# Kernel optimization log

Hardware: AMD Instinct MI355X
Metric: run time of the kernel (lower is better)

## Reference

```python
import jax, jax.numpy as jnp
import numpy as np

LAM = 10.0          # lam_val from __init__ (cp.Constant)
N_ITERS = 100       # fixed FISTA iterations; converges to QP solution (kappa ~ 1+16*LAM)


def _dtd(v):
    """Apply D^T D where D is the (n-2, n) second-difference operator, along last axis."""
    d = v[..., 2:] - 2.0 * v[..., 1:-1] + v[..., :-2]            # D v, shape (..., n-2)
    pad = [(0, 0)] * (v.ndim - 1) + [(2, 2)]
    dp = jnp.pad(d, pad)                                          # zero-pad for adjoint
    return dp[..., 2:] - 2.0 * dp[..., 1:-1] + dp[..., :-2]      # D^T d, shape (..., n)


def _solve_rows(y):
    """Batched QP:  min ||y - x||^2 + LAM * ||diff(x, 2)||^2  s.t.  0 <= x <= y,
    solved independently along the last axis via projected accelerated gradient (FISTA).
    Hessian/2 = I + LAM * D^T D, lambda_max(D^T D) <= 16 -> Lipschitz L = 2*(1 + 16*LAM).
    """
    step = 1.0 / (2.0 * (1.0 + 16.0 * LAM))
    proj = lambda v: jnp.clip(v, 0.0, y)   # box projection onto [0, y]
    x0 = proj(y)

    def body(i, carry):
        x, z, t = carry
        g = 2.0 * (z - y) + (2.0 * LAM) * _dtd(z)
        x_new = proj(z - step * g)
        t_new = 0.5 * (1.0 + jnp.sqrt(1.0 + 4.0 * t * t))
        z_new = x_new + ((t - 1.0) / t_new) * (x_new - x)
        return (x_new, z_new, t_new)

    x, _, _ = jax.lax.fori_loop(0, N_ITERS, body, (x0, x0, jnp.float32(1.0)))
    return x


def setup_inputs() -> dict:
    key = jax.random.key(0)
    # Batch of images in [0,1] (like normalized MNIST); constraint 0 <= x <= y is feasible.
    data = jax.random.uniform(key, (32, 512, 512), dtype=jnp.float32)
    return {"data": data}


def reference(data):
    # Pass 1: denoise each row of each image.
    pass1 = _solve_rows(data)
    # Pass 2: the original call() transposes a numpy VIEW and writes in place, so its
    # "column" pass actually re-solves the SAME rows (with y = pass-1 output) and the
    # final transpose undoes itself. We replicate that exact math.
    pass2 = _solve_rows(pass1)
    b, h, w = pass2.shape
    return pass2.reshape(b, h, w, 1)
```

## Files before the change

### kernel.cpp

```cpp
#include <hip/hip_runtime.h>
#include <math.h>

#define ROW_N 512
#define N_ITERS 100
#define LAMBDA 10.0f

typedef float f2 __attribute__((ext_vector_type(2)));

__device__ __forceinline__ f2 splat(float s) { f2 r; r.x = s; r.y = s; return r; }
__device__ __forceinline__ f2 ffma(f2 a, f2 b, f2 c) {
    return __builtin_elementwise_fma(a, b, c);
}

#define DPP_WAVE_SHL1 0x130
#define DPP_WAVE_SHR1 0x138

template <int CTRL>
__device__ __forceinline__ f2 dpp2(f2 old, f2 src) {
    f2 r;
    r.x = __int_as_float(__builtin_amdgcn_update_dpp(
        __float_as_int(old.x), __float_as_int(src.x), CTRL, 0xF, 0xF, false));
    r.y = __int_as_float(__builtin_amdgcn_update_dpp(
        __float_as_int(old.y), __float_as_int(src.y), CTRL, 0xF, 0xF, false));
    return r;
}

__global__ void coef_kernel(float* __restrict__ coefs) {
    if (threadIdx.x == 0) {
        float t = 1.0f;
        for (int k = 0; k < N_ITERS; ++k) {
            float t_new = 0.5f * (1.0f + sqrtf(1.0f + 4.0f * t * t));
            coefs[k] = (t - 1.0f) / t_new;
            t = t_new;
        }
    }
}

template <bool USE_TABLE>
__global__ __launch_bounds__(256)
__attribute__((amdgpu_waves_per_eu(2, 8)))
void fista_kernel(
    const float* __restrict__ in, float* __restrict__ out,
    const float* __restrict__ coefs, int n_rows)
{
    const int pid  = (int)((blockIdx.x * 256u + threadIdx.x) >> 6);
    const int lane = (int)(threadIdx.x & 63u);
    const int n_pairs = (n_rows + 1) >> 1;
    if (pid >= n_pairs) return;

    const int r0 = pid * 2;
    const int r1 = (r0 + 1 < n_rows) ? r0 + 1 : r0;
    const float* rowA = in + (size_t)r0 * ROW_N + lane * 8;
    const float* rowB = in + (size_t)r1 * ROW_N + lane * 8;

    const float A = 1.0f / (1.0f + 16.0f * LAMBDA);
    const float B = LAMBDA / (1.0f + 16.0f * LAMBDA);
    const float C = 1.0f - A;
    const f2 K0 = splat(C - 6.0f * B);
    const f2 B4 = splat(4.0f * B);
    const f2 Bn = splat(-B);
    const f2 Av = splat(A);
    const f2 TWO = splat(2.0f);

    f2 y[8], ay[8], xA[8], xB[8], z[8];
    {
        const float4 a0 = *(const float4*)(rowA);
        const float4 a1 = *(const float4*)(rowA + 4);
        const float4 b0 = *(const float4*)(rowB);
        const float4 b1 = *(const float4*)(rowB + 4);
        y[0].x = a0.x; y[1].x = a0.y; y[2].x = a0.z; y[3].x = a0.w;
        y[4].x = a1.x; y[5].x = a1.y; y[6].x = a1.z; y[7].x = a1.w;
        y[0].y = b0.x; y[1].y = b0.y; y[2].y = b0.z; y[3].y = b0.w;
        y[4].y = b1.x; y[5].y = b1.y; y[6].y = b1.z; y[7].y = b1.w;
    }

    f2 zm1, zm2, zp0, zp1;

    auto make_halos = [&]() {
        f2 gm1 = ffma(TWO, z[0], -z[1]);
        f2 gm2 = ffma(TWO, gm1, -z[0]);
        f2 gp0 = ffma(TWO, z[7], -z[6]);
        f2 gp1 = ffma(TWO, gp0, -z[7]);
        zm1 = dpp2<DPP_WAVE_SHR1>(gm1, z[7]);
        zm2 = dpp2<DPP_WAVE_SHR1>(gm2, z[6]);
        zp0 = dpp2<DPP_WAVE_SHL1>(gp0, z[0]);
        zp1 = dpp2<DPP_WAVE_SHL1>(gp1, z[1]);
    };

    auto upd = [&](int i, f2 a, f2 b, f2 c, f2 d,
                   const f2* xin, f2* xout, f2 cf) {
        f2 t1 = a + b;
        f2 t2 = c + d;
        f2 u = ffma(K0, z[i], ay[i]);
        u = ffma(B4, t1, u);
        u = ffma(Bn, t2, u);
        f2 xe;
        xe.x = __builtin_amdgcn_fmed3f(u.x, 0.0f, y[i].x);
        xe.y = __builtin_amdgcn_fmed3f(u.y, 0.0f, y[i].y);
        z[i] = ffma(cf, xe - xin[i], xe);
        xout[i] = xe;
    };

    auto step = [&](const f2* xin, f2* xout, float cfs) {
        const f2 cf = splat(cfs);
        f2 o0 = z[0], o1 = z[1], o2 = z[2], o3 = z[3], o4 = z[4],
           o5 = z[5], o6 = z[6];
        upd(0, zm1, z[1], zm2, z[2], xin, xout, cf);
        upd(1, o0,  z[2], zm1, z[3], xin, xout, cf);
        upd(2, o1,  z[3], o0,  z[4], xin, xout, cf);
        upd(3, o2,  z[4], o1,  z[5], xin, xout, cf);
        upd(4, o3,  z[5], o2,  z[6], xin, xout, cf);
        upd(5, o4,  z[6], o3,  z[7], xin, xout, cf);
        upd(6, o5,  z[7], o4,  zp0,  xin, xout, cf);
        upd(7, o6,  zp0,  o5,  zp1,  xin, xout, cf);
        make_halos();
    };

    #pragma unroll 1
    for (int pass = 0; pass < 2; ++pass) {
        #pragma unroll
        for (int i = 0; i < 8; ++i) {
            ay[i] = Av * y[i];
            xA[i] = y[i];
            z[i]  = y[i];
        }
        make_halos();

        float c0, c1, tcur = 1.0f;
        if (USE_TABLE) { c0 = coefs[0]; c1 = coefs[1]; }
        else {
            float tn = 0.5f * (1.0f + sqrtf(fmaf(4.0f * tcur, tcur, 1.0f)));
            c0 = (tcur - 1.0f) / tn;
            float tn2 = 0.5f * (1.0f + sqrtf(fmaf(4.0f * tn, tn, 1.0f)));
            c1 = (tn - 1.0f) / tn2;
            tcur = tn2;
        }

        #pragma unroll 1
        for (int it = 0; it < N_ITERS; it += 2) {
            float n0, n1;
            if (USE_TABLE) {
                const int j = (it + 2 < N_ITERS) ? it + 2 : 0;
                n0 = coefs[j];
                n1 = coefs[j + 1];
            } else {
                float tn = 0.5f * (1.0f + sqrtf(fmaf(4.0f * tcur, tcur, 1.0f)));
                n0 = (tcur - 1.0f) / tn;
                float tn2 = 0.5f * (1.0f + sqrtf(fmaf(4.0f * tn, tn, 1.0f)));
                n1 = (tn - 1.0f) / tn2;
                tcur = tn2;
            }
            step(xA, xB, c0);
            step(xB, xA, c1);
            c0 = n0; c1 = n1;
        }

        if (pass == 0) {
            #pragma unroll
            for (int i = 0; i < 8; ++i) y[i] = xA[i];
        }
    }

    float* orowA = out + (size_t)r0 * ROW_N + lane * 8;
    *(float4*)(orowA)     = make_float4(xA[0].x, xA[1].x, xA[2].x, xA[3].x);
    *(float4*)(orowA + 4) = make_float4(xA[4].x, xA[5].x, xA[6].x, xA[7].x);
    if (r1 > r0) {
        float* orowB = out + (size_t)r1 * ROW_N + lane * 8;
        *(float4*)(orowB)     = make_float4(xA[0].y, xA[1].y, xA[2].y, xA[3].y);
        *(float4*)(orowB + 4) = make_float4(xA[4].y, xA[5].y, xA[6].y, xA[7].y);
    }
}

extern "C" void kernel_launch(void* const* d_in, const int* in_sizes, int n_in,
                              void* d_out, int out_size, void* d_ws, size_t ws_size,
                              hipStream_t stream) {
    const float* in = (const float*)d_in[0];
    float* out = (float*)d_out;

    const int total   = in_sizes[0];
    const int n_rows  = total / ROW_N;
    const int n_pairs = (n_rows + 1) >> 1;
    const int waves_per_block = 4;
    const int blocks = (n_pairs + waves_per_block - 1) / waves_per_block;

    if (ws_size >= N_ITERS * sizeof(float)) {
        float* coefs = (float*)d_ws;
        coef_kernel<<<1, 64, 0, stream>>>(coefs);
        fista_kernel<true><<<blocks, 256, 0, stream>>>(in, out, coefs, n_rows);
    } else {
        fista_kernel<false><<<blocks, 256, 0, stream>>>(in, out, nullptr, n_rows);
    }
}
```

Baseline: 344.8 us.

## Run early FISTA iterations in packed fp16 with momentum form, finish in fp32

Runs the first 68 FISTA iterations per pass in packed half precision on values shifted by -0.5, using a reformulated momentum (v) update and a cascaded difference stencil for D^T D. The last 32 iterations run in fp32 to recover accuracy. The waves-per-EU hint is also raised. The aim is to double arithmetic throughput per instruction and cut register pressure. The risk is fp16 rounding that the fp32 tail may not fully correct, which could break tolerance.

Result: slower. 425.0 us (+23.3%).

```diff
diff --git a/kernel.cpp b/kernel.cpp
--- a/kernel.cpp
+++ b/kernel.cpp
@@ -3,12 +3,21 @@
 
 #define ROW_N 512
 #define N_ITERS 100
+#define N_TAIL_F32 32
+#define N_F16 (N_ITERS - N_TAIL_F32)
 #define LAMBDA 10.0f
 
 typedef float f2 __attribute__((ext_vector_type(2)));
+typedef _Float16 h2 __attribute__((ext_vector_type(2)));
 
 __device__ __forceinline__ f2 splat(float s) { f2 r; r.x = s; r.y = s; return r; }
+__device__ __forceinline__ h2 splat_h(float s) {
+    h2 r; r.x = (_Float16)s; r.y = (_Float16)s; return r;
+}
 __device__ __forceinline__ f2 ffma(f2 a, f2 b, f2 c) {
+    return __builtin_elementwise_fma(a, b, c);
+}
+__device__ __forceinline__ h2 hfma(h2 a, h2 b, h2 c) {
     return __builtin_elementwise_fma(a, b, c);
 }
 
@@ -25,6 +34,14 @@
     return r;
 }
 
+template <int CTRL>
+__device__ __forceinline__ h2 dpp_h2(h2 old, h2 src) {
+    int o = __builtin_bit_cast(int, old);
+    int s = __builtin_bit_cast(int, src);
+    int r = __builtin_amdgcn_update_dpp(o, s, CTRL, 0xF, 0xF, false);
+    return __builtin_bit_cast(h2, r);
+}
+
 __global__ void coef_kernel(float* __restrict__ coefs) {
     if (threadIdx.x == 0) {
         float t = 1.0f;
@@ -38,7 +55,7 @@
 
 template <bool USE_TABLE>
 __global__ __launch_bounds__(256)
-__attribute__((amdgpu_waves_per_eu(2, 8)))
+__attribute__((amdgpu_waves_per_eu(4, 8)))
 void fista_kernel(
     const float* __restrict__ in, float* __restrict__ out,
     const float* __restrict__ coefs, int n_rows)
@@ -53,121 +70,176 @@
     const float* rowA = in + (size_t)r0 * ROW_N + lane * 8;
     const float* rowB = in + (size_t)r1 * ROW_N + lane * 8;
 
-    const float A = 1.0f / (1.0f + 16.0f * LAMBDA);
-    const float B = LAMBDA / (1.0f + 16.0f * LAMBDA);
-    const float C = 1.0f - A;
-    const f2 K0 = splat(C - 6.0f * B);
-    const f2 B4 = splat(4.0f * B);
-    const f2 Bn = splat(-B);
-    const f2 Av = splat(A);
-    const f2 TWO = splat(2.0f);
-
-    f2 y[8], ay[8], xA[8], xB[8], z[8];
+    const float A  = 1.0f / (1.0f + 16.0f * LAMBDA);
+    const float B  = LAMBDA / (1.0f + 16.0f * LAMBDA);
+    const float C  = 1.0f - A;
+    const float K0f = C - 6.0f * B;
+    const float B4f = 4.0f * B;
+    const float Bnf = -B;
+
+    const f2 K0 = splat(K0f), B4 = splat(B4f), Bn = splat(Bnf);
+    const f2 Av = splat(A), TWO = splat(2.0f);
+    const h2 nAh = splat_h(-A), Bnh = splat_h(Bnf);
+    const h2 two_h = splat_h(2.0f), zero_h = splat_h(0.0f);
+    const h2 nhalf_h = splat_h(-0.5f);
+
+    f2 y32[8], ay32[8], x32[8], z32[8];
     {
         const float4 a0 = *(const float4*)(rowA);
         const float4 a1 = *(const float4*)(rowA + 4);
         const float4 b0 = *(const float4*)(rowB);
         const float4 b1 = *(const float4*)(rowB + 4);
-        y[0].x = a0.x; y[1].x = a0.y; y[2].x = a0.z; y[3].x = a0.w;
-        y[4].x = a1.x; y[5].x = a1.y; y[6].x = a1.z; y[7].x = a1.w;
-        y[0].y = b0.x; y[1].y = b0.y; y[2].y = b0.z; y[3].y = b0.w;
-        y[4].y = b1.x; y[5].y = b1.y; y[6].y = b1.z; y[7].y = b1.w;
-    }
-
+        y32[0].x = a0.x; y32[1].x = a0.y; y32[2].x = a0.z; y32[3].x = a0.w;
+        y32[4].x = a1.x; y32[5].x = a1.y; y32[6].x = a1.z; y32[7].x = a1.w;
+        y32[0].y = b0.x; y32[1].y = b0.y; y32[2].y = b0.z; y32[3].y = b0.w;
+        y32[4].y = b1.x; y32[5].y = b1.y; y32[6].y = b1.z; y32[7].y = b1.w;
+    }
+
+    h2 y16[8], ay16[8], x16[8], v16[8];
     f2 zm1, zm2, zp0, zp1;
 
-    auto make_halos = [&]() {
-        f2 gm1 = ffma(TWO, z[0], -z[1]);
-        f2 gm2 = ffma(TWO, gm1, -z[0]);
-        f2 gp0 = ffma(TWO, z[7], -z[6]);
-        f2 gp1 = ffma(TWO, gp0, -z[7]);
-        zm1 = dpp2<DPP_WAVE_SHR1>(gm1, z[7]);
-        zm2 = dpp2<DPP_WAVE_SHR1>(gm2, z[6]);
-        zp0 = dpp2<DPP_WAVE_SHL1>(gp0, z[0]);
-        zp1 = dpp2<DPP_WAVE_SHL1>(gp1, z[1]);
-    };
-
-    auto upd = [&](int i, f2 a, f2 b, f2 c, f2 d,
-                   const f2* xin, f2* xout, f2 cf) {
+    auto step16 = [&](float cfs) {
+        const h2 cf = splat_h(cfs);
+        h2 zz[8];
+        #pragma unroll
+        for (int i = 0; i < 8; ++i) zz[i] = x16[i] + v16[i];
+        h2 gp0 = hfma(two_h, zz[7], -zz[6]);
+        h2 zp0h = dpp_h2<DPP_WAVE_SHL1>(gp0, zz[0]);
+        h2 f[8];
+        #pragma unroll
+        for (int i = 0; i < 7; ++i) f[i] = zz[i + 1] - zz[i];
+        f[7] = zp0h - zz[7];
+        h2 fm1 = dpp_h2<DPP_WAVE_SHR1>(f[0], f[7]);
+        h2 s[8];
+        s[0] = f[0] - fm1;
+        #pragma unroll
+        for (int i = 1; i < 8; ++i) s[i] = f[i] - f[i - 1];
+        h2 s8 = dpp_h2<DPP_WAVE_SHL1>(zero_h, s[0]);
+        h2 g[8];
+        #pragma unroll
+        for (int i = 0; i < 7; ++i) g[i] = s[i + 1] - s[i];
+        g[7] = s8 - s[7];
+        h2 gprev = dpp_h2<DPP_WAVE_SHR1>(zero_h, g[7]);
+        #pragma unroll
+        for (int i = 0; i < 8; ++i) {
+            h2 dd = g[i] - gprev;
+            gprev = g[i];
+            h2 delta = hfma(nAh, zz[i], ay16[i]);
+            delta = hfma(Bnh, dd, delta);
+            h2 sm = v16[i] + delta;
+            h2 u = x16[i] + sm;
+            h2 xe = __builtin_elementwise_min(
+                        __builtin_elementwise_max(u, nhalf_h), y16[i]);
+            h2 d = xe - x16[i];
+            v16[i] = cf * d;
+            x16[i] = xe;
+        }
+    };
+
+    auto make_halos32 = [&]() {
+        f2 gm1 = ffma(TWO, z32[0], -z32[1]);
+        f2 gm2 = ffma(TWO, gm1, -z32[0]);
+        f2 gp0 = ffma(TWO, z32[7], -z32[6]);
+        f2 gp1 = ffma(TWO, gp0, -z32[7]);
+        zm1 = dpp2<DPP_WAVE_SHR1>(gm1, z32[7]);
+        zm2 = dpp2<DPP_WAVE_SHR1>(gm2, z32[6]);
+        zp0 = dpp2<DPP_WAVE_SHL1>(gp0, z32[0]);
+        zp1 = dpp2<DPP_WAVE_SHL1>(gp1, z32[1]);
+    };
+
+    auto upd32 = [&](int i, f2 a, f2 b, f2 c, f2 d, f2 cf) {
         f2 t1 = a + b;
         f2 t2 = c + d;
-        f2 u = ffma(K0, z[i], ay[i]);
+        f2 u = ffma(K0, z32[i], ay32[i]);
         u = ffma(B4, t1, u);
         u = ffma(Bn, t2, u);
         f2 xe;
-        xe.x = __builtin_amdgcn_fmed3f(u.x, 0.0f, y[i].x);
-        xe.y = __builtin_amdgcn_fmed3f(u.y, 0.0f, y[i].y);
-        z[i] = ffma(cf, xe - xin[i], xe);
-        xout[i] = xe;
-    };
-
-    auto step = [&](const f2* xin, f2* xout, float cfs) {
+        xe.x = __builtin_amdgcn_fmed3f(u.x, 0.0f, y32[i].x);
+        xe.y = __builtin_amdgcn_fmed3f(u.y, 0.0f, y32[i].y);
+        z32[i] = ffma(cf, xe - x32[i], xe);
+        x32[i] = xe;
+    };
+
+    auto step32 = [&](float cfs) {
         const f2 cf = splat(cfs);
-        f2 o0 = z[0], o1 = z[1], o2 = z[2], o3 = z[3], o4 = z[4],
-           o5 = z[5], o6 = z[6];
-        upd(0, zm1, z[1], zm2, z[2], xin, xout, cf);
-        upd(1, o0,  z[2], zm1, z[3], xin, xout, cf);
-        upd(2, o1,  z[3], o0,  z[4], xin, xout, cf);
-        upd(3, o2,  z[4], o1,  z[5], xin, xout, cf);
-        upd(4, o3,  z[5], o2,  z[6], xin, xout, cf);
-        upd(5, o4,  z[6], o3,  z[7], xin, xout, cf);
-        upd(6, o5,  z[7], o4,  zp0,  xin, xout, cf);
-        upd(7, o6,  zp0,  o5,  zp1,  xin, xout, cf);
-        make_halos();
+        f2 o0 = z32[0], o1 = z32[1], o2 = z32[2], o3 = z32[3],
+           o4 = z32[4], o5 = z32[5], o6 = z32[6];
+        upd32(0, zm1, z32[1], zm2, z32[2], cf);
+        upd32(1, o0,  z32[2], zm1, z32[3], cf);
+        upd32(2, o1,  z32[3], o0,  z32[4], cf);
+        upd32(3, o2,  z32[4], o1,  z32[5], cf);
+        upd32(4, o3,  z32[5], o2,  z32[6], cf);
+        upd32(5, o4,  z32[6], o3,  z32[7], cf);
+        upd32(6, o5,  z32[7], o4,  zp0,   cf);
+        upd32(7, o6,  zp0,    o5,  zp1,   cf);
+        make_halos32();
+    };
+
+    auto next_coef = [](float& t) {
+        float tn = 0.5f * (1.0f + sqrtf(fmaf(4.0f * t, t, 1.0f)));
+        float c = (t - 1.0f) / tn;
+        t = tn;
+        return c;
     };
 
     #pragma unroll 1
     for (int pass = 0; pass < 2; ++pass) {
         #pragma unroll
         for (int i = 0; i < 8; ++i) {
-            ay[i] = Av * y[i];
-            xA[i] = y[i];
-            z[i]  = y[i];
-        }
-        make_halos();
-
-        float c0, c1, tcur = 1.0f;
-        if (USE_TABLE) { c0 = coefs[0]; c1 = coefs[1]; }
-        else {
-            float tn = 0.5f * (1.0f + sqrtf(fmaf(4.0f * tcur, tcur, 1.0f)));
-            c0 = (tcur - 1.0f) / tn;
-            float tn2 = 0.5f * (1.0f + sqrtf(fmaf(4.0f * tn, tn, 1.0f)));
-            c1 = (tn - 1.0f) / tn2;
-            tcur = tn2;
-        }
+            float ypx = y32[i].x - 0.5f, ypy = y32[i].y - 0.5f;
+            h2 yv; yv.x = (_Float16)ypx; yv.y = (_Float16)ypy;
+            h2 av; av.x = (_Float16)(A * ypx); av.y = (_Float16)(A * ypy);
+            y16[i]  = yv;
+            ay16[i] = av;
+            x16[i]  = yv;
+            v16[i]  = splat_h(0.0f);
+        }
+
+        float t_run = 1.0f;
+        float c_cur = USE_TABLE ? coefs[0] : next_coef(t_run);
 
         #pragma unroll 1
-        for (int it = 0; it < N_ITERS; it += 2) {
-            float n0, n1;
+        for (int it = 0; it < N_F16; ++it) {
+            float c_nxt = USE_TABLE ? coefs[it + 1] : next_coef(t_run);
+            step16(c_cur);
+            c_cur = c_nxt;
+        }
+
+        #pragma unroll
+        for (int i = 0; i < 8; ++i) {
+            float xx = (float)x16[i].x + 0.5f, xy = (float)x16[i].y + 0.5f;
+            x32[i].x = xx;                     x32[i].y = xy;
+            z32[i].x = xx + (float)v16[i].x;   z32[i].y = xy + (float)v16[i].y;
+            ay32[i] = Av * y32[i];
+        }
+        make_halos32();
+
+        #pragma unroll 1
+        for (int it = N_F16; it < N_ITERS; ++it) {
+            float c_nxt;
             if (USE_TABLE) {
-                const int j = (it + 2 < N_ITERS) ? it + 2 : 0;
-                n0 = coefs[j];
-                n1 = coefs[j + 1];
+                const int j = (it + 1 < N_ITERS) ? it + 1 : 0;
+                c_nxt = coefs[j];
             } else {
-                float tn = 0.5f * (1.0f + sqrtf(fmaf(4.0f * tcur, tcur, 1.0f)));
-                n0 = (tcur - 1.0f) / tn;
-                float tn2 = 0.5f * (1.0f + sqrtf(fmaf(4.0f * tn, tn, 1.0f)));
-                n1 = (tn - 1.0f) / tn2;
-                tcur = tn2;
+                c_nxt = next_coef(t_run);
             }
-            step(xA, xB, c0);
-            step(xB, xA, c1);
-            c0 = n0; c1 = n1;
+            step32(c_cur);
+            c_cur = c_nxt;
         }
 
         if (pass == 0) {
             #pragma unroll
-            for (int i = 0; i < 8; ++i) y[i] = xA[i];
+            for (int i = 0; i < 8; ++i) y32[i] = x32[i];
         }
     }
 
     float* orowA = out + (size_t)r0 * ROW_N + lane * 8;
-    *(float4*)(orowA)     = make_float4(xA[0].x, xA[1].x, xA[2].x, xA[3].x);
-    *(float4*)(orowA + 4) = make_float4(xA[4].x, xA[5].x, xA[6].x, xA[7].x);
+    *(float4*)(orowA)     = make_float4(x32[0].x, x32[1].x, x32[2].x, x32[3].x);
+    *(float4*)(orowA + 4) = make_float4(x32[4].x, x32[5].x, x32[6].x, x32[7].x);
     if (r1 > r0) {
         float* orowB = out + (size_t)r1 * ROW_N + lane * 8;
-        *(float4*)(orowB)     = make_float4(xA[0].y, xA[1].y, xA[2].y, xA[3].y);
-        *(float4*)(orowB + 4) = make_float4(xA[4].y, xA[5].y, xA[6].y, xA[7].y);
+        *(float4*)(orowB)     = make_float4(x32[0].y, x32[1].y, x32[2].y, x32[3].y);
+        *(float4*)(orowB + 4) = make_float4(x32[4].y, x32[5].y, x32[6].y, x32[7].y);
     }
 }
 
@@ -183,7 +255,7 @@
     const int waves_per_block = 4;
     const int blocks = (n_pairs + waves_per_block - 1) / waves_per_block;
 
-    if (ws_size >= N_ITERS * sizeof(float)) {
+    if (ws_size >= (N_ITERS + 1) * sizeof(float)) {
         float* coefs = (float*)d_ws;
         coef_kernel<<<1, 64, 0, stream>>>(coefs);
         fista_kernel<true><<<blocks, 256, 0, stream>>>(in, out, coefs, n_rows);
```
